# Kernel optimization log

Measured on AMD Instinct MI355X. Metric: run time of the kernel, lower is better.

The kernel has to match this reference:

```python
import jax, jax.numpy as jnp
import numpy as np

N = 100000   # nodes
E = 1600000  # edges
D = 64       # in = hidden channels
L = 4        # num_layers
G = 512      # graphs in batch
OUT = 10     # out_channels
EPS = 1e-5   # batch-norm eps


def setup_inputs() -> dict:
    key = jax.random.key(0)
    ks = jax.random.split(key, 10)
    x = jax.random.normal(ks[0], (N, D), jnp.float32)
    edge_index = jax.random.randint(ks[1], (2, E), 0, N, dtype=jnp.int32)
    batch = jnp.sort(jax.random.randint(ks[2], (N,), 0, G, dtype=jnp.int32))
    Ws = jax.random.normal(ks[3], (L, D, D), jnp.float32) * 0.1   # GCNConv weights
    bs = jax.random.normal(ks[4], (L, D), jnp.float32) * 0.01     # GCNConv biases
    W1 = jax.random.normal(ks[5], (L * D, D), jnp.float32) * 0.1  # MLP hidden lin
    b1 = jnp.zeros((D,), jnp.float32)
    gamma = jnp.ones((D,), jnp.float32)   # MLP BatchNorm affine
    beta = jnp.zeros((D,), jnp.float32)
    W2 = jax.random.normal(ks[6], (D, OUT), jnp.float32) * 0.1    # MLP out lin
    b2 = jnp.zeros((OUT,), jnp.float32)
    return {"x": x, "edge_index": edge_index, "batch": batch, "Ws": Ws, "bs": bs,
            "W1": W1, "b1": b1, "gamma": gamma, "beta": beta, "W2": W2, "b2": b2}


def reference(x, edge_index, batch, Ws, bs, W1, b1, gamma, beta, W2, b2):
    src, dst = edge_index[0], edge_index[1]
    # symmetric GCN normalization with self-loops (improved=False -> weight 1)
    deg = jax.ops.segment_sum(jnp.ones((E,), x.dtype), dst, num_segments=N) + 1.0
    dis = jax.lax.rsqrt(deg)                 # deg^{-1/2}, finite since deg >= 1
    enorm = dis[src] * dis[dst]              # per-edge coefficient
    snorm = dis * dis                        # self-loop coefficient

    h = x
    pooled = []
    for l in range(L):  # no activation between convs, as in the source
        hw = h @ Ws[l]                                                   # [N, D]
        agg = jax.ops.segment_sum(hw[src] * enorm[:, None], dst, num_segments=N)
        h = agg + hw * snorm[:, None] + bs[l]
        pooled.append(jax.ops.segment_sum(h, batch, num_segments=G))     # [G, D]
    z = jnp.concatenate(pooled, axis=1)                                  # [G, L*D]

    # PyG MLP([L*D, D, OUT], act='relu'): lin -> batch_norm -> relu -> lin
    z = z @ W1 + b1
    mean = z.mean(axis=0)
    var = z.var(axis=0)
    z = (z - mean) * jax.lax.rsqrt(var + EPS) * gamma + beta
    z = jax.nn.relu(z)
    return z @ W2 + b2
```

## Files before the change

### kernel.cpp

```cpp
#include <hip/hip_runtime.h>

#define NN   100000
#define NE   1600000
#define DD   64
#define LL   4
#define GG   512
#define OUTC 10
#define EPSV 1e-5f
#define PARTSZ 12500
#define CAP   250000

#define OFF_RS    0
#define OFF_CSR   100016
#define OFF_BUFA  1700016
#define OFF_BUFB  8100016
#define OFF_POOL  14500016

static __device__ __forceinline__ unsigned short f2bf(float f) {
    unsigned int u = __float_as_uint(f);
    unsigned int r = (u + 0x7fffu + ((u >> 16) & 1u)) >> 16;
    return (unsigned short)r;
}
static __device__ __forceinline__ float plo(unsigned int v) {
    return __uint_as_float(v << 16);
}
static __device__ __forceinline__ float phi(unsigned int v) {
    return __uint_as_float(v & 0xffff0000u);
}

__global__ __launch_bounds__(256)
void bucket_kernel(const int* __restrict__ src, const int* __restrict__ dst,
                   int* __restrict__ bucketCnt, unsigned int* __restrict__ staging) {
    __shared__ int hist[8];
    __shared__ int base[8];
    int tid = threadIdx.x;
    if (tid < 8) hist[tid] = 0;
    __syncthreads();
    int e0 = blockIdx.x * 1024 + tid * 4;
    int b0 = 0, b1 = 0, b2 = 0, b3 = 0, p0 = 0, p1 = 0, p2 = 0, p3 = 0;
    unsigned int k0 = 0, k1 = 0, k2 = 0, k3 = 0;
    bool ok = (e0 < NE);
    if (ok) {
        int4 d4 = *(const int4*)&dst[e0];
        int4 s4 = *(const int4*)&src[e0];
        b0 = d4.x / PARTSZ; k0 = ((unsigned int)(d4.x - b0 * PARTSZ) << 17) | (unsigned int)s4.x;
        b1 = d4.y / PARTSZ; k1 = ((unsigned int)(d4.y - b1 * PARTSZ) << 17) | (unsigned int)s4.y;
        b2 = d4.z / PARTSZ; k2 = ((unsigned int)(d4.z - b2 * PARTSZ) << 17) | (unsigned int)s4.z;
        b3 = d4.w / PARTSZ; k3 = ((unsigned int)(d4.w - b3 * PARTSZ) << 17) | (unsigned int)s4.w;
        p0 = atomicAdd(&hist[b0], 1);
        p1 = atomicAdd(&hist[b1], 1);
        p2 = atomicAdd(&hist[b2], 1);
        p3 = atomicAdd(&hist[b3], 1);
    }
    __syncthreads();
    if (tid < 8) base[tid] = atomicAdd(&bucketCnt[tid], hist[tid]);
    __syncthreads();
    if (ok) {
        staging[b0 * CAP + base[b0] + p0] = k0;
        staging[b1 * CAP + base[b1] + p1] = k1;
        staging[b2 * CAP + base[b2] + p2] = k2;
        staging[b3 * CAP + base[b3] + p3] = k3;
    }
}

__global__ __launch_bounds__(256)
void deg_bucket_kernel(const unsigned int* __restrict__ staging,
                       const int* __restrict__ bucketCnt, int* __restrict__ deg) {
    int b   = blockIdx.x & 7;
    int sub = blockIdx.x >> 3;
    int nb  = gridDim.x >> 3;
    int cnt = bucketCnt[b];
    const unsigned int* st = staging + b * CAP;
    int dbase = b * PARTSZ;
    for (int i = sub * 256 + threadIdx.x; i < cnt; i += nb * 256) {
        unsigned int v = st[i];
        atomicAdd(&deg[dbase + (v >> 17)], 1);
    }
}

__global__ void scan1_kernel(const int* __restrict__ deg, int* __restrict__ loc,
                             int* __restrict__ bsum) {
    int t = threadIdx.x;
    int i = blockIdx.x * 1024 + t;
    int v = (i < NN) ? deg[i] : 0;
    __shared__ int ps[1024];
    ps[t] = v;
    __syncthreads();
    #pragma unroll
    for (int off = 1; off < 1024; off <<= 1) {
        int u = (t >= off) ? ps[t - off] : 0;
        __syncthreads();
        ps[t] += u;
        __syncthreads();
    }
    if (i < NN) loc[i] = ps[t] - v;
    if (t == 1023) bsum[blockIdx.x] = ps[1023];
}

__global__ void scan2_kernel(const int* __restrict__ bsum, int* __restrict__ boff) {
    int t = threadIdx.x;
    int v = (t < 98) ? bsum[t] : 0;
    __shared__ int ps[128];
    ps[t] = v;
    __syncthreads();
    #pragma unroll
    for (int off = 1; off < 128; off <<= 1) {
        int u = (t >= off) ? ps[t - off] : 0;
        __syncthreads();
        ps[t] += u;
        __syncthreads();
    }
    if (t < 98) boff[t] = ps[t] - v;
    if (t == 127) boff[98] = ps[127];
}

__global__ void scan3_kernel(const int* __restrict__ loc, const int* __restrict__ boff,
                             int* __restrict__ rs) {
    int i = blockIdx.x * 1024 + threadIdx.x;
    if (i < NN) rs[i] = loc[i] + boff[i >> 10];
    if (i == NN) rs[NN] = boff[98];
}

__global__ __launch_bounds__(256)
void fill_bucket_kernel(const unsigned int* __restrict__ staging,
                        const int* __restrict__ bucketCnt, const int* __restrict__ rs,
                        int* __restrict__ cnt, int* __restrict__ csr) {
    int b   = blockIdx.x & 7;
    int sub = blockIdx.x >> 3;
    int nb  = gridDim.x >> 3;
    int n   = bucketCnt[b];
    const unsigned int* st = staging + b * CAP;
    int dbase = b * PARTSZ;
    for (int i = sub * 256 + threadIdx.x; i < n; i += nb * 256) {
        unsigned int v = st[i];
        int d = dbase + (int)(v >> 17);
        int slot = rs[d] + atomicAdd(&cnt[d], 1);
        csr[slot] = (int)(v & 0x1FFFFu);
    }
}

__global__ void t0_kernel(const float* __restrict__ x, const int* __restrict__ rs,
                          unsigned short* __restrict__ t0) {
    int i = blockIdx.x * 256 + threadIdx.x;
    int n = i >> 4;
    float di = rsqrtf((float)(rs[n + 1] - rs[n]) + 1.0f);
    float4 v = ((const float4*)x)[i];
    ushort4 o;
    o.x = f2bf(v.x * di); o.y = f2bf(v.y * di);
    o.z = f2bf(v.z * di); o.w = f2bf(v.w * di);
    ((ushort4*)t0)[i] = o;
}

__global__ __launch_bounds__(256)
void gather_kernel(const unsigned short* __restrict__ t, const int* __restrict__ csr,
                   const int* __restrict__ rs, unsigned short* __restrict__ vout) {
    const uint2* tu2 = (const uint2*)t;
    uint2* vo2 = (uint2*)vout;
    int tid = threadIdx.x;
    int nwg = gridDim.x;
    int q = nwg >> 3, r = nwg & 7;
    int xcd = blockIdx.x & 7, sub = blockIdx.x >> 3;
    int bid = (xcd < r ? xcd * (q + 1) : r * (q + 1) + (xcd - r) * q) + sub;

    int n = bid * 16 + (tid >> 4);
    int l = tid & 15;
    int j0 = rs[n], j1 = rs[n + 1];
    float di = rsqrtf((float)(j1 - j0) + 1.0f);

    uint2 sv = tu2[n * 16 + l];
    float a0 = plo(sv.x), a1 = phi(sv.x), a2 = plo(sv.y), a3 = phi(sv.y);

    int j = j0;
    #pragma clang loop unroll(disable)
    for (; j + 7 < j1; j += 8) {
        int i0 = csr[j],     i1 = csr[j + 1], i2 = csr[j + 2], i3 = csr[j + 3];
        int i4 = csr[j + 4], i5 = csr[j + 5], i6 = csr[j + 6], i7 = csr[j + 7];
        uint2 v0 = tu2[i0 * 16 + l];
        uint2 v1 = tu2[i1 * 16 + l];
        uint2 v2 = tu2[i2 * 16 + l];
        uint2 v3 = tu2[i3 * 16 + l];
        uint2 v4 = tu2[i4 * 16 + l];
        uint2 v5 = tu2[i5 * 16 + l];
        uint2 v6 = tu2[i6 * 16 + l];
        uint2 v7 = tu2[i7 * 16 + l];
        a0 += ((plo(v0.x) + plo(v1.x)) + (plo(v2.x) + plo(v3.x)))
            + ((plo(v4.x) + plo(v5.x)) + (plo(v6.x) + plo(v7.x)));
        a1 += ((phi(v0.x) + phi(v1.x)) + (phi(v2.x) + phi(v3.x)))
            + ((phi(v4.x) + phi(v5.x)) + (phi(v6.x) + phi(v7.x)));
        a2 += ((plo(v0.y) + plo(v1.y)) + (plo(v2.y) + plo(v3.y)))
            + ((plo(v4.y) + plo(v5.y)) + (plo(v6.y) + plo(v7.y)));
        a3 += ((phi(v0.y) + phi(v1.y)) + (phi(v2.y) + phi(v3.y)))
            + ((phi(v4.y) + phi(v5.y)) + (phi(v6.y) + phi(v7.y)));
    }
    #pragma clang loop unroll(disable)
    for (; j + 3 < j1; j += 4) {
        int i0 = csr[j], i1 = csr[j + 1], i2 = csr[j + 2], i3 = csr[j + 3];
        uint2 v0 = tu2[i0 * 16 + l];
        uint2 v1 = tu2[i1 * 16 + l];
        uint2 v2 = tu2[i2 * 16 + l];
        uint2 v3 = tu2[i3 * 16 + l];
        a0 += (plo(v0.x) + plo(v1.x)) + (plo(v2.x) + plo(v3.x));
        a1 += (phi(v0.x) + phi(v1.x)) + (phi(v2.x) + phi(v3.x));
        a2 += (plo(v0.y) + plo(v1.y)) + (plo(v2.y) + plo(v3.y));
        a3 += (phi(v0.y) + phi(v1.y)) + (phi(v2.y) + phi(v3.y));
    }
    #pragma clang loop unroll(disable)
    for (; j < j1; ++j) {
        uint2 v0 = tu2[csr[j] * 16 + l];
        a0 += plo(v0.x); a1 += phi(v0.x);
        a2 += plo(v0.y); a3 += phi(v0.y);
    }
    uint2 o;
    o.x = (unsigned int)f2bf(a0 * di) | ((unsigned int)f2bf(a1 * di) << 16);
    o.y = (unsigned int)f2bf(a2 * di) | ((unsigned int)f2bf(a3 * di) << 16);
    vo2[n * 16 + l] = o;
}

__global__ __launch_bounds__(256)
void vgemm_kernel(const unsigned short* __restrict__ v, const float* __restrict__ W,
                  const float* __restrict__ bias, const int* __restrict__ rs,
                  const int* __restrict__ batch, unsigned short* __restrict__ tout,
                  float* __restrict__ pooled, int l, int last) {
    __shared__ float Wsh[64 * 64];
    __shared__ float hs[16][64];
    __shared__ float red[4][64];
    const uint2* vu2 = (const uint2*)v;
    int tid = threadIdx.x;
    #pragma unroll
    for (int i = 0; i < 16; ++i) Wsh[tid + i * 256] = W[tid + i * 256];
    int w = tid >> 6, d = tid & 63;
    float bd = bias[d];

    for (int c = blockIdx.x; c < NN / 16; c += gridDim.x) {
        int n0 = c * 16;
        {
            int rr = tid >> 4, cc = tid & 15;
            uint2 u = vu2[(n0 + rr) * 16 + cc];
            hs[rr][4 * cc]     = plo(u.x);
            hs[rr][4 * cc + 1] = phi(u.x);
            hs[rr][4 * cc + 2] = plo(u.y);
            hs[rr][4 * cc + 3] = phi(u.y);
        }
        __syncthreads();
        float a0 = 0.f, a1 = 0.f, a2 = 0.f, a3 = 0.f;
        #pragma unroll 2
        for (int k4 = 0; k4 < 16; ++k4) {
            float4 h0 = *(const float4*)&hs[w * 4 + 0][k4 * 4];
            float4 h1 = *(const float4*)&hs[w * 4 + 1][k4 * 4];
            float4 h2 = *(const float4*)&hs[w * 4 + 2][k4 * 4];
            float4 h3 = *(const float4*)&hs[w * 4 + 3][k4 * 4];
            float w0 = Wsh[(k4 * 4 + 0) * 64 + d];
            float w1 = Wsh[(k4 * 4 + 1) * 64 + d];
            float w2 = Wsh[(k4 * 4 + 2) * 64 + d];
            float w3 = Wsh[(k4 * 4 + 3) * 64 + d];
            a0 = fmaf(h0.x, w0, a0); a0 = fmaf(h0.y, w1, a0);
            a0 = fmaf(h0.z, w2, a0); a0 = fmaf(h0.w, w3, a0);
            a1 = fmaf(h1.x, w0, a1); a1 = fmaf(h1.y, w1, a1);
            a1 = fmaf(h1.z, w2, a1); a1 = fmaf(h1.w, w3, a1);
            a2 = fmaf(h2.x, w0, a2); a2 = fmaf(h2.y, w1, a2);
            a2 = fmaf(h2.z, w2, a2); a2 = fmaf(h2.w, w3, a2);
            a3 = fmaf(h3.x, w0, a3); a3 = fmaf(h3.y, w1, a3);
            a3 = fmaf(h3.z, w2, a3); a3 = fmaf(h3.w, w3, a3);
        }
        float accs[4] = {a0, a1, a2, a3};
        if (!last) {
            #pragma unroll
            for (int s = 0; s < 4; ++s) {
                int n = n0 + w * 4 + s;
                float di = rsqrtf((float)(rs[n + 1] - rs[n]) + 1.0f);
                tout[n * 64 + d] = f2bf((accs[s] + bd) * di);
            }
        }
        int glo = batch[n0], ghi = batch[n0 + 15];
        if (glo == ghi) {
            red[w][d] = ((a0 + a1) + (a2 + a3)) + 4.0f * bd;
            __syncthreads();
            if (w == 0) {
                float tot = (red[0][d] + red[1][d]) + (red[2][d] + red[3][d]);
                atomicAdd(&pooled[glo * 256 + l * 64 + d], tot);
            }
        } else {
            #pragma unroll
            for (int s = 0; s < 4; ++s) {
                int n = n0 + w * 4 + s;
                atomicAdd(&pooled[batch[n] * 256 + l * 64 + d], accs[s] + bd);
            }
        }
        __syncthreads();
    }
}

__global__ void mlp1_kernel(const float* __restrict__ pooled, const float* __restrict__ W1,
                            const float* __restrict__ b1, float* __restrict__ z1,
                            float* __restrict__ sums) {
    __shared__ float row[256];
    int g = blockIdx.x, d = threadIdx.x;
    #pragma unroll
    for (int i = 0; i < 4; ++i) row[d + i * 64] = pooled[g * 256 + d + i * 64];
    __syncthreads();
    float acc = b1[d];
    #pragma unroll 8
    for (int k = 0; k < 256; ++k) acc = fmaf(row[k], W1[k * 64 + d], acc);
    z1[g * 64 + d] = acc;
    atomicAdd(&sums[d], acc);
    atomicAdd(&sums[64 + d], acc * acc);
}

__global__ void mlp2_kernel(const float* __restrict__ z1, const float* __restrict__ sums,
                            const float* __restrict__ gamma, const float* __restrict__ beta,
                            const float* __restrict__ W2, const float* __restrict__ b2,
                            float* __restrict__ out) {
    int g = blockIdx.x, d = threadIdx.x;
    float mean = sums[d] * (1.0f / 512.0f);
    float var  = sums[64 + d] * (1.0f / 512.0f) - mean * mean;
    float z = (z1[g * 64 + d] - mean) * rsqrtf(var + EPSV) * gamma[d] + beta[d];
    z = fmaxf(z, 0.0f);
    #pragma unroll
    for (int o = 0; o < OUTC; ++o) {
        float v = z * W2[d * OUTC + o];
        #pragma unroll
        for (int s = 32; s; s >>= 1) v += __shfl_xor(v, s, 64);
        if (d == 0) out[g * OUTC + o] = v + b2[o];
    }
}

extern "C" void kernel_launch(void* const* d_in, const int* in_sizes, int n_in,
                              void* d_out, int out_size, void* d_ws, size_t ws_size,
                              hipStream_t stream) {
    (void)in_sizes; (void)n_in; (void)out_size; (void)ws_size;
    const float* x     = (const float*)d_in[0];
    const int*   ei    = (const int*)d_in[1];
    const int*   src   = ei;
    const int*   dst   = ei + NE;
    const int*   batch = (const int*)d_in[2];
    const float* Wc    = (const float*)d_in[3];
    const float* bc    = (const float*)d_in[4];
    const float* W1    = (const float*)d_in[5];
    const float* b1    = (const float*)d_in[6];
    const float* gamma = (const float*)d_in[7];
    const float* beta  = (const float*)d_in[8];
    const float* W2    = (const float*)d_in[9];
    const float* b2    = (const float*)d_in[10];
    float* out = (float*)d_out;
    float* ws  = (float*)d_ws;

    int*   rs        = (int*)(ws + OFF_RS);
    int*   bucketCnt = (int*)(ws + OFF_RS) + 100004;
    int*   csr       = (int*)(ws + OFF_CSR);
    int*   loc       = (int*)(ws + OFF_CSR);
    unsigned short* tping = (unsigned short*)(ws + OFF_BUFA);
    unsigned short* vbuf  = tping + 6400000;
    unsigned short* tpong = (unsigned short*)(ws + OFF_BUFB);
    unsigned int* staging = (unsigned int*)(ws + OFF_BUFB);
    float* pooled = ws + OFF_POOL;
    int*   degcnt = (int*)(ws + OFF_POOL);
    int*   bsum   = (int*)(ws + OFF_BUFA);
    int*   boff   = (int*)(ws + OFF_BUFA) + 128;
    float* z1     = ws + OFF_BUFA;
    float* sums   = ws + OFF_BUFA + GG * DD;

    hipMemsetAsync(bucketCnt, 0, 8 * sizeof(int), stream);
    hipMemsetAsync(degcnt, 0, NN * sizeof(int), stream);
    bucket_kernel<<<(NE + 1023) / 1024, 256, 0, stream>>>(src, dst, bucketCnt, staging);
    deg_bucket_kernel<<<1024, 256, 0, stream>>>(staging, bucketCnt, degcnt);
    scan1_kernel<<<98, 1024, 0, stream>>>(degcnt, loc, bsum);
    scan2_kernel<<<1, 128, 0, stream>>>(bsum, boff);
    scan3_kernel<<<99, 1024, 0, stream>>>(loc, boff, rs);
    hipMemsetAsync(degcnt, 0, NN * sizeof(int), stream);
    fill_bucket_kernel<<<1024, 256, 0, stream>>>(staging, bucketCnt, rs, degcnt, csr);

    t0_kernel<<<NN * 16 / 256, 256, 0, stream>>>(x, rs, tping);
    hipMemsetAsync(pooled, 0, GG * LL * DD * sizeof(float), stream);

    unsigned short* tin = tping; unsigned short* tot = tpong;
    for (int l = 0; l < LL; ++l) {
        gather_kernel<<<NN / 16, 256, 0, stream>>>(tin, csr, rs, vbuf);
        vgemm_kernel<<<768, 256, 0, stream>>>(vbuf, Wc + l * 4096, bc + l * 64,
                                              rs, batch, tot, pooled,
                                              l, l == LL - 1);
        unsigned short* tmp = tin; tin = tot; tot = tmp;
    }

    hipMemsetAsync(sums, 0, 128 * sizeof(float), stream);
    mlp1_kernel<<<GG, 64, 0, stream>>>(pooled, W1, b1, z1, sums);
    mlp2_kernel<<<GG, 64, 0, stream>>>(z1, sums, gamma, beta, W2, b2, out);
}
```

Measured before the change: 519.5 us.

## Replace global-atomic degree count and CSR fill with LDS sub-range histograms

Degree counting and CSR placement now assign each block a sub-range of about 390 destination nodes within a bucket and use shared-memory histograms and counters instead of global atomics. This removes two memsets and the contention of global atomics. In exchange, every block rescans its entire bucket (32x redundant reads of the staging array, about 200K entries each), so global traffic grows considerably.

```diff
diff --git a/kernel.cpp b/kernel.cpp
--- a/kernel.cpp
+++ b/kernel.cpp
@@ -8,6 +8,7 @@
 #define OUTC 10
 #define EPSV 1e-5f
 #define PARTSZ 12500
+#define SUBS   32
 #define CAP   250000
 
 #define OFF_RS    0
@@ -63,19 +64,27 @@
     }
 }
 
-__global__ __launch_bounds__(256)
-void deg_bucket_kernel(const unsigned int* __restrict__ staging,
-                       const int* __restrict__ bucketCnt, int* __restrict__ deg) {
-    int b   = blockIdx.x & 7;
-    int sub = blockIdx.x >> 3;
-    int nb  = gridDim.x >> 3;
+__global__ __launch_bounds__(512)
+void count_sub_kernel(const unsigned int* __restrict__ staging,
+                      const int* __restrict__ bucketCnt, int* __restrict__ deg) {
+    __shared__ int hist[392];
+    int b   = blockIdx.x >> 5;
+    int sub = blockIdx.x & 31;
+    int lo  = (sub * PARTSZ) / SUBS;
+    int hi  = ((sub + 1) * PARTSZ) / SUBS;
+    int nloc = hi - lo;
+    int tid = threadIdx.x;
+    for (int i = tid; i < nloc; i += 512) hist[i] = 0;
+    __syncthreads();
     int cnt = bucketCnt[b];
     const unsigned int* st = staging + b * CAP;
-    int dbase = b * PARTSZ;
-    for (int i = sub * 256 + threadIdx.x; i < cnt; i += nb * 256) {
-        unsigned int v = st[i];
-        atomicAdd(&deg[dbase + (v >> 17)], 1);
-    }
+    for (int i = tid; i < cnt; i += 512) {
+        int d = (int)(st[i] >> 17);
+        if (d >= lo && d < hi) atomicAdd(&hist[d - lo], 1);
+    }
+    __syncthreads();
+    int dbase = b * PARTSZ + lo;
+    for (int i = tid; i < nloc; i += 512) deg[dbase + i] = hist[i];
 }
 
 __global__ void scan1_kernel(const int* __restrict__ deg, int* __restrict__ loc,
@@ -121,21 +130,29 @@
     if (i == NN) rs[NN] = boff[98];
 }
 
-__global__ __launch_bounds__(256)
-void fill_bucket_kernel(const unsigned int* __restrict__ staging,
-                        const int* __restrict__ bucketCnt, const int* __restrict__ rs,
-                        int* __restrict__ cnt, int* __restrict__ csr) {
-    int b   = blockIdx.x & 7;
-    int sub = blockIdx.x >> 3;
-    int nb  = gridDim.x >> 3;
-    int n   = bucketCnt[b];
+__global__ __launch_bounds__(512)
+void place_sub_kernel(const unsigned int* __restrict__ staging,
+                      const int* __restrict__ bucketCnt, const int* __restrict__ rs,
+                      int* __restrict__ csr) {
+    __shared__ int cnt[392];
+    int b   = blockIdx.x >> 5;
+    int sub = blockIdx.x & 31;
+    int lo  = (sub * PARTSZ) / SUBS;
+    int hi  = ((sub + 1) * PARTSZ) / SUBS;
+    int nloc = hi - lo;
+    int tid = threadIdx.x;
+    for (int i = tid; i < nloc; i += 512) cnt[i] = 0;
+    __syncthreads();
+    int n = bucketCnt[b];
     const unsigned int* st = staging + b * CAP;
-    int dbase = b * PARTSZ;
-    for (int i = sub * 256 + threadIdx.x; i < n; i += nb * 256) {
+    int dbase = b * PARTSZ + lo;
+    for (int i = tid; i < n; i += 512) {
         unsigned int v = st[i];
-        int d = dbase + (int)(v >> 17);
-        int slot = rs[d] + atomicAdd(&cnt[d], 1);
-        csr[slot] = (int)(v & 0x1FFFFu);
+        int d = (int)(v >> 17);
+        if (d >= lo && d < hi) {
+            int slot = rs[dbase + (d - lo)] + atomicAdd(&cnt[d - lo], 1);
+            csr[slot] = (int)(v & 0x1FFFFu);
+        }
     }
 }
 
@@ -353,21 +370,19 @@
     unsigned short* tpong = (unsigned short*)(ws + OFF_BUFB);
     unsigned int* staging = (unsigned int*)(ws + OFF_BUFB);
     float* pooled = ws + OFF_POOL;
-    int*   degcnt = (int*)(ws + OFF_POOL);
+    int*   deg    = (int*)(ws + OFF_POOL);
     int*   bsum   = (int*)(ws + OFF_BUFA);
     int*   boff   = (int*)(ws + OFF_BUFA) + 128;
     float* z1     = ws + OFF_BUFA;
     float* sums   = ws + OFF_BUFA + GG * DD;
 
     hipMemsetAsync(bucketCnt, 0, 8 * sizeof(int), stream);
-    hipMemsetAsync(degcnt, 0, NN * sizeof(int), stream);
     bucket_kernel<<<(NE + 1023) / 1024, 256, 0, stream>>>(src, dst, bucketCnt, staging);
-    deg_bucket_kernel<<<1024, 256, 0, stream>>>(staging, bucketCnt, degcnt);
-    scan1_kernel<<<98, 1024, 0, stream>>>(degcnt, loc, bsum);
+    count_sub_kernel<<<256, 512, 0, stream>>>(staging, bucketCnt, deg);
+    scan1_kernel<<<98, 1024, 0, stream>>>(deg, loc, bsum);
     scan2_kernel<<<1, 128, 0, stream>>>(bsum, boff);
     scan3_kernel<<<99, 1024, 0, stream>>>(loc, boff, rs);
-    hipMemsetAsync(degcnt, 0, NN * sizeof(int), stream);
-    fill_bucket_kernel<<<1024, 256, 0, stream>>>(staging, bucketCnt, rs, degcnt, csr);
+    place_sub_kernel<<<256, 512, 0, stream>>>(staging, bucketCnt, rs, csr);
 
     t0_kernel<<<NN * 16 / 256, 256, 0, stream>>>(x, rs, tping);
     hipMemsetAsync(pooled, 0, GG * LL * DD * sizeof(float), stream);
```

After: 664.2 us. +27.8%, slower.

## Partition edges into 256 fine buckets and build CSR with shared-memory histograms

Applied to the files above, without the earlier changes.

Edges are now bucketed by destination into 256 partitions of 391 nodes instead of 8 partitions of 12500. With partitions that small, one block can own each partition, so degree counting and CSR slot placement use shared-memory atomics instead of global atomics. This drops two memsets and the global count array. The cost is far fewer blocks (256) for the count and place passes, and a per-bucket capacity of 8192 that could overflow on skewed inputs.

```diff
diff --git a/kernel.cpp b/kernel.cpp
--- a/kernel.cpp
+++ b/kernel.cpp
@@ -7,8 +7,8 @@
 #define GG   512
 #define OUTC 10
 #define EPSV 1e-5f
-#define PARTSZ 12500
-#define CAP   250000
+#define PART  391
+#define CAP   8192
 
 #define OFF_RS    0
 #define OFF_CSR   100016
@@ -31,10 +31,10 @@
 __global__ __launch_bounds__(256)
 void bucket_kernel(const int* __restrict__ src, const int* __restrict__ dst,
                    int* __restrict__ bucketCnt, unsigned int* __restrict__ staging) {
-    __shared__ int hist[8];
-    __shared__ int base[8];
-    int tid = threadIdx.x;
-    if (tid < 8) hist[tid] = 0;
+    __shared__ int hist[256];
+    __shared__ int base[256];
+    int tid = threadIdx.x;
+    hist[tid] = 0;
     __syncthreads();
     int e0 = blockIdx.x * 1024 + tid * 4;
     int b0 = 0, b1 = 0, b2 = 0, b3 = 0, p0 = 0, p1 = 0, p2 = 0, p3 = 0;
@@ -43,17 +43,17 @@
     if (ok) {
         int4 d4 = *(const int4*)&dst[e0];
         int4 s4 = *(const int4*)&src[e0];
-        b0 = d4.x / PARTSZ; k0 = ((unsigned int)(d4.x - b0 * PARTSZ) << 17) | (unsigned int)s4.x;
-        b1 = d4.y / PARTSZ; k1 = ((unsigned int)(d4.y - b1 * PARTSZ) << 17) | (unsigned int)s4.y;
-        b2 = d4.z / PARTSZ; k2 = ((unsigned int)(d4.z - b2 * PARTSZ) << 17) | (unsigned int)s4.z;
-        b3 = d4.w / PARTSZ; k3 = ((unsigned int)(d4.w - b3 * PARTSZ) << 17) | (unsigned int)s4.w;
+        b0 = d4.x / PART; k0 = ((unsigned int)(d4.x - b0 * PART) << 17) | (unsigned int)s4.x;
+        b1 = d4.y / PART; k1 = ((unsigned int)(d4.y - b1 * PART) << 17) | (unsigned int)s4.y;
+        b2 = d4.z / PART; k2 = ((unsigned int)(d4.z - b2 * PART) << 17) | (unsigned int)s4.z;
+        b3 = d4.w / PART; k3 = ((unsigned int)(d4.w - b3 * PART) << 17) | (unsigned int)s4.w;
         p0 = atomicAdd(&hist[b0], 1);
         p1 = atomicAdd(&hist[b1], 1);
         p2 = atomicAdd(&hist[b2], 1);
         p3 = atomicAdd(&hist[b3], 1);
     }
     __syncthreads();
-    if (tid < 8) base[tid] = atomicAdd(&bucketCnt[tid], hist[tid]);
+    base[tid] = atomicAdd(&bucketCnt[tid], hist[tid]);
     __syncthreads();
     if (ok) {
         staging[b0 * CAP + base[b0] + p0] = k0;
@@ -64,18 +64,20 @@
 }
 
 __global__ __launch_bounds__(256)
-void deg_bucket_kernel(const unsigned int* __restrict__ staging,
-                       const int* __restrict__ bucketCnt, int* __restrict__ deg) {
-    int b   = blockIdx.x & 7;
-    int sub = blockIdx.x >> 3;
-    int nb  = gridDim.x >> 3;
+void count_kernel(const unsigned int* __restrict__ staging,
+                  const int* __restrict__ bucketCnt, int* __restrict__ deg) {
+    __shared__ int hist[PART];
+    int b = blockIdx.x;
+    int tid = threadIdx.x;
+    for (int i = tid; i < PART; i += 256) hist[i] = 0;
+    __syncthreads();
     int cnt = bucketCnt[b];
     const unsigned int* st = staging + b * CAP;
-    int dbase = b * PARTSZ;
-    for (int i = sub * 256 + threadIdx.x; i < cnt; i += nb * 256) {
-        unsigned int v = st[i];
-        atomicAdd(&deg[dbase + (v >> 17)], 1);
-    }
+    for (int i = tid; i < cnt; i += 256) atomicAdd(&hist[st[i] >> 17], 1);
+    __syncthreads();
+    int dbase = b * PART;
+    for (int i = tid; i < PART; i += 256)
+        if (dbase + i < NN) deg[dbase + i] = hist[i];
 }
 
 __global__ void scan1_kernel(const int* __restrict__ deg, int* __restrict__ loc,
@@ -122,19 +124,21 @@
 }
 
 __global__ __launch_bounds__(256)
-void fill_bucket_kernel(const unsigned int* __restrict__ staging,
-                        const int* __restrict__ bucketCnt, const int* __restrict__ rs,
-                        int* __restrict__ cnt, int* __restrict__ csr) {
-    int b   = blockIdx.x & 7;
-    int sub = blockIdx.x >> 3;
-    int nb  = gridDim.x >> 3;
-    int n   = bucketCnt[b];
+void place_kernel(const unsigned int* __restrict__ staging,
+                  const int* __restrict__ bucketCnt, const int* __restrict__ rs,
+                  int* __restrict__ csr) {
+    __shared__ int cnt[PART];
+    int b = blockIdx.x;
+    int tid = threadIdx.x;
+    for (int i = tid; i < PART; i += 256) cnt[i] = 0;
+    __syncthreads();
+    int n = bucketCnt[b];
     const unsigned int* st = staging + b * CAP;
-    int dbase = b * PARTSZ;
-    for (int i = sub * 256 + threadIdx.x; i < n; i += nb * 256) {
+    int dbase = b * PART;
+    for (int i = tid; i < n; i += 256) {
         unsigned int v = st[i];
-        int d = dbase + (int)(v >> 17);
-        int slot = rs[d] + atomicAdd(&cnt[d], 1);
+        int dloc = (int)(v >> 17);
+        int slot = rs[dbase + dloc] + atomicAdd(&cnt[dloc], 1);
         csr[slot] = (int)(v & 0x1FFFFu);
     }
 }
@@ -345,7 +349,6 @@
     float* ws  = (float*)d_ws;
 
     int*   rs        = (int*)(ws + OFF_RS);
-    int*   bucketCnt = (int*)(ws + OFF_RS) + 100004;
     int*   csr       = (int*)(ws + OFF_CSR);
     int*   loc       = (int*)(ws + OFF_CSR);
     unsigned short* tping = (unsigned short*)(ws + OFF_BUFA);
@@ -353,21 +356,20 @@
     unsigned short* tpong = (unsigned short*)(ws + OFF_BUFB);
     unsigned int* staging = (unsigned int*)(ws + OFF_BUFB);
     float* pooled = ws + OFF_POOL;
-    int*   degcnt = (int*)(ws + OFF_POOL);
+    int*   deg       = (int*)(ws + OFF_POOL);
+    int*   bucketCnt = (int*)(ws + OFF_POOL) + NN;
     int*   bsum   = (int*)(ws + OFF_BUFA);
     int*   boff   = (int*)(ws + OFF_BUFA) + 128;
     float* z1     = ws + OFF_BUFA;
     float* sums   = ws + OFF_BUFA + GG * DD;
 
-    hipMemsetAsync(bucketCnt, 0, 8 * sizeof(int), stream);
-    hipMemsetAsync(degcnt, 0, NN * sizeof(int), stream);
+    hipMemsetAsync(bucketCnt, 0, 256 * sizeof(int), stream);
     bucket_kernel<<<(NE + 1023) / 1024, 256, 0, stream>>>(src, dst, bucketCnt, staging);
-    deg_bucket_kernel<<<1024, 256, 0, stream>>>(staging, bucketCnt, degcnt);
-    scan1_kernel<<<98, 1024, 0, stream>>>(degcnt, loc, bsum);
+    count_kernel<<<256, 256, 0, stream>>>(staging, bucketCnt, deg);
+    scan1_kernel<<<98, 1024, 0, stream>>>(deg, loc, bsum);
     scan2_kernel<<<1, 128, 0, stream>>>(bsum, boff);
     scan3_kernel<<<99, 1024, 0, stream>>>(loc, boff, rs);
-    hipMemsetAsync(degcnt, 0, NN * sizeof(int), stream);
-    fill_bucket_kernel<<<1024, 256, 0, stream>>>(staging, bucketCnt, rs, degcnt, csr);
+    place_kernel<<<256, 256, 0, stream>>>(staging, bucketCnt, rs, csr);
 
     t0_kernel<<<NN * 16 / 256, 256, 0, stream>>>(x, rs, tping);
     hipMemsetAsync(pooled, 0, GG * LL * DD * sizeof(float), stream);
```

New measurement: 423.7 us. 1.23x faster.
